# Kernel tuning notes

Hardware: AMD Instinct MI355X
Metric: run time of the kernel (lower is better)

## Reference

```python
import jax, jax.numpy as jnp
import numpy as np

B = 32          # batch_size
M = 1024        # mesh_num (nodes per sub-graph)
D_IN = 128      # sub_node_feature_input_dim
D_OUT = 128     # sub_node_feature_output_dim
E_DIM = 64      # embedding dim per node


def setup_inputs() -> dict:
    key = jax.random.key(0)
    k1, k2, k3, k4 = jax.random.split(key, 4)
    return {
        "node_feature_group": jax.random.normal(k1, (B * M, D_IN), dtype=jnp.float32),
        "embedding_group": jax.random.normal(k2, (B * M, E_DIM), dtype=jnp.float32),
        "W1": jax.random.normal(k3, (D_OUT, D_IN), dtype=jnp.float32) * (1.0 / np.sqrt(D_IN)),
        "W2": jax.random.normal(k4, (D_OUT, D_OUT), dtype=jnp.float32) * (1.0 / np.sqrt(D_OUT)),
    }


def reference(node_feature_group, embedding_group, W1, W2):
    # The torch module builds a (B*M)x(B*M) block-diagonal adjacency via
    # torch.block_diag; off-block entries are exactly zero, and row sums /
    # D^-1/2 A D^-1/2 normalization act per block, so we compute per-graph.
    E = embedding_group.reshape(B, M, E_DIM)
    adj = jnp.maximum(jnp.einsum('bme,bne->bmn', E, E), 0.0)  # clamp(E E^T, 0)
    adj = adj + jnp.eye(M, dtype=adj.dtype)                   # A = adj + I
    d = adj.sum(-1)                                           # [B, M]
    dinv = d ** -0.5                                          # symmetric=True
    dad = dinv[:, :, None] * adj * dinv[:, None, :]           # D^-1/2 A D^-1/2

    X = node_feature_group.reshape(B, M, D_IN)
    y = jax.nn.relu(jnp.einsum('bmn,bnd->bmd', dad, X) @ W1.T)   # gcn1
    y = jax.nn.relu(jnp.einsum('bmn,bnd->bmd', dad, y) @ W2.T)   # gcn2
    # Dropout is identity in eval mode.
    return y.reshape(B * M, D_OUT)
```

## Files before the change

### kernel.cpp

```cpp
#include <hip/hip_runtime.h>
#include <stdint.h>

#define B_  32
#define M_  1024
#define DF  128
#define ED  64

typedef __attribute__((ext_vector_type(8))) short short8;
typedef __attribute__((ext_vector_type(4))) short short4v;
typedef __attribute__((ext_vector_type(4))) float floatx4;

__device__ inline unsigned short f2bf(float f) {
    union { float f; unsigned u; } v; v.f = f;
    unsigned r = v.u + 0x7fffu + ((v.u >> 16) & 1u);
    return (unsigned short)(r >> 16);
}

__device__ inline short8 cvt8(float4 a, float4 b) {
    short8 s;
    s[0] = (short)f2bf(a.x); s[1] = (short)f2bf(a.y);
    s[2] = (short)f2bf(a.z); s[3] = (short)f2bf(a.w);
    s[4] = (short)f2bf(b.x); s[5] = (short)f2bf(b.y);
    s[6] = (short)f2bf(b.z); s[7] = (short)f2bf(b.w);
    return s;
}

__device__ inline void remap_block(int& b, int& mt2) {
    int lin = blockIdx.y * 16 + blockIdx.x;
    int g = lin & 7, kk = lin >> 3;
    b = g * 4 + (kk >> 4);
    mt2 = kk & 15;
}

__global__ __launch_bounds__(256) void prep_kernel(
    const float* __restrict__ E, const float* __restrict__ X,
    unsigned short* __restrict__ Ebf, float* __restrict__ dinv,
    unsigned short* __restrict__ Xt) {
    int b, mt2; remap_block(b, mt2);
    int m0 = mt2 * 64;
    int t = threadIdx.x;
    int w = t >> 6, lane = t & 63, quad = lane >> 4, lc = lane & 15;

    __shared__ unsigned short sEn[128 * 72];
    __shared__ float sDinv[64];

    const float* Eb = E + (size_t)b * M_ * ED;
    unsigned short* Ebg = Ebf + (size_t)b * M_ * ED;
    int base_m = m0 + w * 16;

    short8 afr[2];
    for (int ks = 0; ks < 2; ++ks) {
        const float* p = Eb + (size_t)(base_m + lc) * ED + ks * 32 + quad * 8;
        afr[ks] = cvt8(*(const float4*)p, *(const float4*)(p + 4));
    }
    floatx4 rsum = (floatx4){0.f, 0.f, 0.f, 0.f};

    for (int nc = 0; nc < 8; ++nc) {
        __syncthreads();
        for (int it = 0; it < 4; ++it) {
            int c = t + 256 * it;
            int row = c >> 3, off = (c & 7) * 8;
            const float* p = Eb + (size_t)(nc * 128 + row) * ED + off;
            *(short8*)(&sEn[row * 72 + off]) = cvt8(*(const float4*)p, *(const float4*)(p + 4));
        }
        __syncthreads();
        if ((mt2 & 7) == nc) {
            int half = mt2 >> 3;
            for (int it = 0; it < 2; ++it) {
                int c = t + 256 * it;
                int row = half * 64 + (c >> 3), off = (c & 7) * 8;
                *(short8*)(Ebg + (size_t)(nc * 128 + row) * ED + off) =
                    *(const short8*)(&sEn[row * 72 + off]);
            }
        }
        for (int nt = 0; nt < 8; ++nt) {
            short8 b0 = *(const short8*)(&sEn[(nt * 16 + lc) * 72 + quad * 8]);
            short8 b1 = *(const short8*)(&sEn[(nt * 16 + lc) * 72 + 32 + quad * 8]);
            floatx4 s = (floatx4){0.f, 0.f, 0.f, 0.f};
            s = __builtin_amdgcn_mfma_f32_16x16x32_bf16(afr[0], b0, s, 0, 0, 0);
            s = __builtin_amdgcn_mfma_f32_16x16x32_bf16(afr[1], b1, s, 0, 0, 0);
            int n = nc * 128 + nt * 16 + lc;
            for (int r = 0; r < 4; ++r) {
                int m = base_m + quad * 4 + r;
                float v = fmaxf(s[r], 0.f);
                if (m == n) v += 1.0f;
                rsum[r] += v;
            }
        }
    }
    for (int r = 0; r < 4; ++r) {
        float v = rsum[r];
        v += __shfl_xor(v, 1, 16);
        v += __shfl_xor(v, 2, 16);
        v += __shfl_xor(v, 4, 16);
        v += __shfl_xor(v, 8, 16);
        if (lc == 0) {
            float dvv = rsqrtf(v);
            int mloc = w * 16 + quad * 4 + r;
            sDinv[mloc] = dvv;
            dinv[b * M_ + m0 + mloc] = dvv;
        }
    }
    __syncthreads();
    {
        int nloc = t >> 5;
        int d4 = (t & 31) * 4;
        for (int pass = 0; pass < 8; ++pass) {
            int n = pass * 8 + nloc;
            float sc = sDinv[n];
            float4 v = *(const float4*)(X + (size_t)(b * M_ + m0 + n) * DF + d4);
            sEn[(d4 + 0) * 72 + n] = f2bf(v.x * sc);
            sEn[(d4 + 1) * 72 + n] = f2bf(v.y * sc);
            sEn[(d4 + 2) * 72 + n] = f2bf(v.z * sc);
            sEn[(d4 + 3) * 72 + n] = f2bf(v.w * sc);
        }
    }
    __syncthreads();
    for (int it = 0; it < 4; ++it) {
        int c = t + 256 * it;
        int d = c >> 3, off = (c & 7) * 8;
        *(short8*)(Xt + (size_t)(b * DF + d) * M_ + m0 + off) =
            *(const short8*)(&sEn[d * 72 + off]);
    }
}

template <int MODE>
__global__ __launch_bounds__(256) void layer_kernel(
    const unsigned short* __restrict__ Ebf,
    const unsigned short* __restrict__ Pt,
    const float* __restrict__ Wf,
    const float* __restrict__ dinv,
    unsigned short* __restrict__ OutT,
    float* __restrict__ OutF) {
    int b, mt2; remap_block(b, mt2);
    int m0 = mt2 * 64;
    int t = threadIdx.x;
    int w = t >> 6, lane = t & 63, quad = lane >> 4, lc = lane & 15;
    int wr = w & 1, wc = w >> 1;

    __shared__ unsigned short lds[35328];
    unsigned short* sEn = lds;
    unsigned short* sS  = lds + 9216;
    unsigned short* sPW = lds + 17920;

    const unsigned short* Eb = Ebf + (size_t)b * M_ * ED;
    const unsigned short* Pb = Pt + (size_t)b * DF * M_;

    short8 ae[2][2];
    for (int i = 0; i < 2; ++i) {
        int row = m0 + wr * 32 + i * 16 + lc;
        for (int ks = 0; ks < 2; ++ks)
            ae[i][ks] = *(const short8*)(Eb + (size_t)row * ED + ks * 32 + quad * 8);
    }

    floatx4 acc[2][4];
    for (int i = 0; i < 2; ++i)
        for (int j = 0; j < 4; ++j) acc[i][j] = (floatx4){0.f, 0.f, 0.f, 0.f};

    for (int nc = 0; nc < 8; ++nc) {
        __syncthreads();
        for (int it = 0; it < 4; ++it) {
            int c = t + 256 * it;
            int row = c >> 3, off = (c & 7) * 8;
            *(short8*)(&sEn[row * 72 + off]) =
                *(const short8*)(Eb + (size_t)(nc * 128 + row) * ED + off);
        }
        for (int it = 0; it < 8; ++it) {
            int c = t + 256 * it;
            int drow = c >> 4, off = (c & 15) * 8;
            *(short8*)(&sPW[drow * 136 + off]) =
                *(const short8*)(Pb + (size_t)drow * M_ + nc * 128 + off);
        }
        __syncthreads();
        for (int jt = 0; jt < 4; ++jt) {
            int ncol = wc * 64 + jt * 16;
            short8 b0 = *(const short8*)(&sEn[(ncol + lc) * 72 + quad * 8]);
            short8 b1 = *(const short8*)(&sEn[(ncol + lc) * 72 + 32 + quad * 8]);
            for (int i = 0; i < 2; ++i) {
                floatx4 s = (floatx4){0.f, 0.f, 0.f, 0.f};
                s = __builtin_amdgcn_mfma_f32_16x16x32_bf16(ae[i][0], b0, s, 0, 0, 0);
                s = __builtin_amdgcn_mfma_f32_16x16x32_bf16(ae[i][1], b1, s, 0, 0, 0);
                int mrow = wr * 32 + i * 16 + quad * 4;
                for (int r = 0; r < 4; ++r) {
                    float v = fmaxf(s[r], 0.f);
                    if (m0 + mrow + r == nc * 128 + ncol + lc) v += 1.0f;
                    sS[(mrow + r) * 136 + ncol + lc] = f2bf(v);
                }
            }
        }
        __syncthreads();
        for (int ks = 0; ks < 4; ++ks) {
            short8 afr[2], bfr[4];
            for (int i = 0; i < 2; ++i)
                afr[i] = *(const short8*)(&sS[(wr * 32 + i * 16 + lc) * 136 + ks * 32 + quad * 8]);
            for (int j = 0; j < 4; ++j)
                bfr[j] = *(const short8*)(&sPW[(wc * 64 + j * 16 + lc) * 136 + ks * 32 + quad * 8]);
            for (int i = 0; i < 2; ++i)
                for (int j = 0; j < 4; ++j)
                    acc[i][j] = __builtin_amdgcn_mfma_f32_16x16x32_bf16(afr[i], bfr[j], acc[i][j], 0, 0, 0);
        }
    }

    float dv[2][4];
    for (int i = 0; i < 2; ++i)
        for (int r = 0; r < 4; ++r)
            dv[i][r] = dinv[b * M_ + m0 + wr * 32 + i * 16 + quad * 4 + r];
    __syncthreads();
    unsigned short* sY = sS;
    unsigned short* sW = sPW;
    for (int i = 0; i < 2; ++i)
        for (int j = 0; j < 4; ++j) {
            int mrow = wr * 32 + i * 16 + quad * 4;
            int col = wc * 64 + j * 16 + lc;
            for (int r = 0; r < 4; ++r)
                sY[(mrow + r) * 136 + col] = f2bf(acc[i][j][r] * dv[i][r]);
        }
    for (int it = 0; it < 8; ++it) {
        int c = t + 256 * it;
        int row = c >> 4, off = (c & 15) * 8;
        const float* p = Wf + row * DF + off;
        *(short8*)(&sW[row * 136 + off]) = cvt8(*(const float4*)p, *(const float4*)(p + 4));
    }
    __syncthreads();
    floatx4 accH[2][4];
    for (int i = 0; i < 2; ++i)
        for (int j = 0; j < 4; ++j) accH[i][j] = (floatx4){0.f, 0.f, 0.f, 0.f};
    for (int ks = 0; ks < 4; ++ks) {
        short8 afr[2], bfr[4];
        for (int i = 0; i < 2; ++i)
            afr[i] = *(const short8*)(&sY[(wr * 32 + i * 16 + lc) * 136 + ks * 32 + quad * 8]);
        for (int j = 0; j < 4; ++j)
            bfr[j] = *(const short8*)(&sW[(wc * 64 + j * 16 + lc) * 136 + ks * 32 + quad * 8]);
        for (int i = 0; i < 2; ++i)
            for (int j = 0; j < 4; ++j)
                accH[i][j] = __builtin_amdgcn_mfma_f32_16x16x32_bf16(afr[i], bfr[j], accH[i][j], 0, 0, 0);
    }
    if (MODE == 2) {
        __syncthreads();
        float* sF = (float*)lds;
        for (int i = 0; i < 2; ++i)
            for (int j = 0; j < 4; ++j) {
                int mrow = wr * 32 + i * 16 + quad * 4;
                int col = wc * 64 + j * 16 + lc;
                for (int r = 0; r < 4; ++r)
                    sF[(mrow + r) * 132 + col] = fmaxf(accH[i][j][r], 0.f);
            }
        __syncthreads();
        float* Ob = OutF + ((size_t)b * M_ + m0) * DF;
        for (int it = 0; it < 8; ++it) {
            int c = t + 256 * it;
            int row = c >> 5, off = (c & 31) * 4;
            *(float4*)(Ob + (size_t)row * DF + off) = *(const float4*)(&sF[row * 132 + off]);
        }
    } else {
        __syncthreads();
        unsigned short* sT = sW;
        for (int i = 0; i < 2; ++i)
            for (int j = 0; j < 4; ++j) {
                int mrow = wr * 32 + i * 16 + quad * 4;
                int col = wc * 64 + j * 16 + lc;
                short4v pk;
                for (int r = 0; r < 4; ++r)
                    pk[r] = (short)f2bf(fmaxf(accH[i][j][r], 0.f) * dv[i][r]);
                *(short4v*)(&sT[col * 72 + mrow]) = pk;
            }
        __syncthreads();
        for (int it = 0; it < 4; ++it) {
            int c = t + 256 * it;
            int o = c >> 3, off = (c & 7) * 8;
            *(short8*)(OutT + (size_t)(b * DF + o) * M_ + m0 + off) =
                *(const short8*)(&sT[o * 72 + off]);
        }
    }
}

__global__ __launch_bounds__(256) void cast_kernel(
    const float* __restrict__ E, const float* __restrict__ W1,
    const float* __restrict__ W2, unsigned short* __restrict__ Ebf,
    unsigned short* __restrict__ W1bf, unsigned short* __restrict__ W2bf) {
    const int NE = B_ * M_ * ED;
    const int NW = DF * DF;
    int idx = (blockIdx.x * 256 + threadIdx.x) * 4;
    const float* src; unsigned short* dst; int off;
    if (idx < NE)            { src = E;  dst = Ebf;  off = idx; }
    else if (idx < NE + NW)  { src = W1; dst = W1bf; off = idx - NE; }
    else                     { src = W2; dst = W2bf; off = idx - NE - NW; }
    float4 v = *(const float4*)(src + off);
    ushort4 o;
    o.x = f2bf(v.x); o.y = f2bf(v.y); o.z = f2bf(v.z); o.w = f2bf(v.w);
    *(ushort4*)(dst + off) = o;
}

__global__ __launch_bounds__(256) void degree_kernel(
    const unsigned short* __restrict__ Ebf, float* __restrict__ dinv) {
    int mt = blockIdx.x, b = blockIdx.y;
    int t = threadIdx.x;
    int w = t >> 6, lane = t & 63, quad = lane >> 4, lc = lane & 15;
    __shared__ unsigned short sEn[128][72];
    const unsigned short* Eb = Ebf + (size_t)b * M_ * ED;
    short8 afr[2][2];
    for (int i = 0; i < 2; ++i) {
        int row = mt * 128 + w * 32 + i * 16 + lc;
        for (int ks = 0; ks < 2; ++ks)
            afr[i][ks] = *(const short8*)(Eb + (size_t)row * ED + ks * 32 + quad * 8);
    }
    floatx4 rsum[2];
    rsum[0] = (floatx4){0.f,0.f,0.f,0.f};
    rsum[1] = (floatx4){0.f,0.f,0.f,0.f};
    for (int nc = 0; nc < 8; ++nc) {
        __syncthreads();
        for (int it = 0; it < 4; ++it) {
            int c = t + 256 * it;
            int row = c >> 3, off = (c & 7) * 8;
            *(short8*)(&sEn[row][off]) =
                *(const short8*)(Eb + (size_t)(nc * 128 + row) * ED + off);
        }
        __syncthreads();
        for (int nt = 0; nt < 8; ++nt) {
            short8 b0 = *(const short8*)(&sEn[nt * 16 + lc][quad * 8]);
            short8 b1 = *(const short8*)(&sEn[nt * 16 + lc][32 + quad * 8]);
            for (int i = 0; i < 2; ++i) {
                floatx4 s = (floatx4){0.f,0.f,0.f,0.f};
                s = __builtin_amdgcn_mfma_f32_16x16x32_bf16(afr[i][0], b0, s, 0, 0, 0);
                s = __builtin_amdgcn_mfma_f32_16x16x32_bf16(afr[i][1], b1, s, 0, 0, 0);
                for (int r = 0; r < 4; ++r) rsum[i][r] += fmaxf(s[r], 0.f);
            }
        }
    }
    for (int i = 0; i < 2; ++i)
        for (int r = 0; r < 4; ++r) {
            float v = rsum[i][r];
            v += __shfl_xor(v, 1, 16);
            v += __shfl_xor(v, 2, 16);
            v += __shfl_xor(v, 4, 16);
            v += __shfl_xor(v, 8, 16);
            if (lc == 0) {
                int row = mt * 128 + w * 32 + i * 16 + quad * 4 + r;
                dinv[b * M_ + row] = rsqrtf(1.0f + v);
            }
        }
}

__global__ __launch_bounds__(256) void tscale128_kernel(
    const float* __restrict__ X, const float* __restrict__ dinv,
    unsigned short* __restrict__ Xt) {
    int mt = blockIdx.x, b = blockIdx.y;
    int t = threadIdx.x;
    __shared__ unsigned short sT[128][136];
    int nloc = t >> 5;
    int d4 = (t & 31) * 4;
    for (int pass = 0; pass < 16; ++pass) {
        int n = pass * 8 + nloc;
        int grow = b * M_ + mt * 128 + n;
        float sc = dinv[grow];
        float4 v = *(const float4*)(X + (size_t)grow * DF + d4);
        sT[d4 + 0][n] = f2bf(v.x * sc);
        sT[d4 + 1][n] = f2bf(v.y * sc);
        sT[d4 + 2][n] = f2bf(v.z * sc);
        sT[d4 + 3][n] = f2bf(v.w * sc);
    }
    __syncthreads();
    for (int it = 0; it < 8; ++it) {
        int c = t + 256 * it;
        int d = c >> 4, off = (c & 15) * 8;
        *(short8*)(Xt + (size_t)(b * DF + d) * M_ + mt * 128 + off) =
            *(const short8*)(&sT[d][off]);
    }
}

template <int MODE>
__global__ __launch_bounds__(256) void gcn_kernel(
    const unsigned short* __restrict__ Ebf,
    const unsigned short* __restrict__ Pt,
    const unsigned short* __restrict__ Wbf,
    const float* __restrict__ dinv,
    unsigned short* __restrict__ OutT,
    float* __restrict__ OutF) {
    int mt = blockIdx.x, b = blockIdx.y;
    int t = threadIdx.x;
    int w = t >> 6, lane = t & 63, quad = lane >> 4, lc = lane & 15;
    int wr = w & 1, wc = w >> 1;
    __shared__ unsigned short sEn[128][72];
    __shared__ unsigned short sS[128][136];
    __shared__ unsigned short sPW[128][136];
    const unsigned short* Eb = Ebf + (size_t)b * M_ * ED;
    short8 ae[4][2];
    for (int i = 0; i < 4; ++i) {
        int row = mt * 128 + wr * 64 + i * 16 + lc;
        for (int ks = 0; ks < 2; ++ks)
            ae[i][ks] = *(const short8*)(Eb + (size_t)row * ED + ks * 32 + quad * 8);
    }
    floatx4 accZ[4][4];
    for (int i = 0; i < 4; ++i)
        for (int j = 0; j < 4; ++j) accZ[i][j] = (floatx4){0.f,0.f,0.f,0.f};
    for (int nc = 0; nc < 8; ++nc) {
        __syncthreads();
        for (int it = 0; it < 4; ++it) {
            int c = t + 256 * it;
            int row = c >> 3, off = (c & 7) * 8;
            *(short8*)(&sEn[row][off]) =
                *(const short8*)(Eb + (size_t)(nc * 128 + row) * ED + off);
        }
        for (int it = 0; it < 8; ++it) {
            int c = t + 256 * it;
            int drow = c >> 4, off = (c & 15) * 8;
            *(short8*)(&sPW[drow][off]) =
                *(const short8*)(Pt + (size_t)(b * DF + drow) * M_ + nc * 128 + off);
        }
        __syncthreads();
        for (int jt = 0; jt < 4; ++jt) {
            int ncol = wc * 64 + jt * 16;
            short8 b0 = *(const short8*)(&sEn[ncol + lc][quad * 8]);
            short8 b1 = *(const short8*)(&sEn[ncol + lc][32 + quad * 8]);
            for (int i = 0; i < 4; ++i) {
                floatx4 s = (floatx4){0.f,0.f,0.f,0.f};
                s = __builtin_amdgcn_mfma_f32_16x16x32_bf16(ae[i][0], b0, s, 0, 0, 0);
                s = __builtin_amdgcn_mfma_f32_16x16x32_bf16(ae[i][1], b1, s, 0, 0, 0);
                int mrow = wr * 64 + i * 16 + quad * 4;
                for (int r = 0; r < 4; ++r) {
                    float v = fmaxf(s[r], 0.f);
                    if (mt == nc && (mrow + r) == (ncol + lc)) v += 1.0f;
                    sS[mrow + r][ncol + lc] = f2bf(v);
                }
            }
        }
        __syncthreads();
        for (int ks = 0; ks < 4; ++ks) {
            short8 afr[4];
            for (int i = 0; i < 4; ++i)
                afr[i] = *(const short8*)(&sS[wr * 64 + i * 16 + lc][ks * 32 + quad * 8]);
            for (int j = 0; j < 4; ++j) {
                short8 bfr = *(const short8*)(&sPW[wc * 64 + j * 16 + lc][ks * 32 + quad * 8]);
                for (int i = 0; i < 4; ++i)
                    accZ[i][j] = __builtin_amdgcn_mfma_f32_16x16x32_bf16(afr[i], bfr, accZ[i][j], 0, 0, 0);
            }
        }
    }
    float dv[4][4];
    for (int i = 0; i < 4; ++i)
        for (int r = 0; r < 4; ++r)
            dv[i][r] = dinv[b * M_ + mt * 128 + wr * 64 + i * 16 + quad * 4 + r];
    __syncthreads();
    for (int i = 0; i < 4; ++i)
        for (int j = 0; j < 4; ++j) {
            int mrow = wr * 64 + i * 16 + quad * 4;
            int col = wc * 64 + j * 16 + lc;
            for (int r = 0; r < 4; ++r)
                sS[mrow + r][col] = f2bf(accZ[i][j][r] * dv[i][r]);
        }
    for (int it = 0; it < 8; ++it) {
        int c = t + 256 * it;
        int row = c >> 4, off = (c & 15) * 8;
        *(short8*)(&sPW[row][off]) = *(const short8*)(Wbf + row * DF + off);
    }
    __syncthreads();
    floatx4 accH[4][4];
    for (int i = 0; i < 4; ++i)
        for (int j = 0; j < 4; ++j) accH[i][j] = (floatx4){0.f,0.f,0.f,0.f};
    for (int ks = 0; ks < 4; ++ks) {
        short8 afr[4], bfr[4];
        for (int i = 0; i < 4; ++i)
            afr[i] = *(const short8*)(&sS[wr * 64 + i * 16 + lc][ks * 32 + quad * 8]);
        for (int j = 0; j < 4; ++j)
            bfr[j] = *(const short8*)(&sPW[wc * 64 + j * 16 + lc][ks * 32 + quad * 8]);
        for (int i = 0; i < 4; ++i)
            for (int j = 0; j < 4; ++j)
                accH[i][j] = __builtin_amdgcn_mfma_f32_16x16x32_bf16(afr[i], bfr[j], accH[i][j], 0, 0, 0);
    }
    if (MODE == 2) {
        float* Ob = OutF + ((size_t)b * M_ + mt * 128) * DF;
        for (int i = 0; i < 4; ++i)
            for (int j = 0; j < 4; ++j) {
                int mrow = wr * 64 + i * 16 + quad * 4;
                int col = wc * 64 + j * 16 + lc;
                for (int r = 0; r < 4; ++r)
                    Ob[(size_t)(mrow + r) * DF + col] = fmaxf(accH[i][j][r], 0.f);
            }
    } else {
        __syncthreads();
        for (int i = 0; i < 4; ++i)
            for (int j = 0; j < 4; ++j) {
                int mrow = wr * 64 + i * 16 + quad * 4;
                int col = wc * 64 + j * 16 + lc;
                for (int r = 0; r < 4; ++r)
                    sS[col][mrow + r] = f2bf(fmaxf(accH[i][j][r], 0.f) * dv[i][r]);
            }
        __syncthreads();
        unsigned short* Ob = OutT + (size_t)b * DF * M_ + mt * 128;
        for (int it = 0; it < 8; ++it) {
            int c = t + 256 * it;
            int orow = c >> 4, off = (c & 15) * 8;
            *(short8*)(Ob + (size_t)orow * M_ + off) = *(const short8*)(&sS[orow][off]);
        }
    }
}

extern "C" void kernel_launch(void* const* d_in, const int* in_sizes, int n_in,
                              void* d_out, int out_size, void* d_ws, size_t ws_size,
                              hipStream_t stream) {
    (void)in_sizes; (void)n_in; (void)out_size;
    const float* X  = (const float*)d_in[0];
    const float* E  = (const float*)d_in[1];
    const float* W1 = (const float*)d_in[2];
    const float* W2 = (const float*)d_in[3];
    float* out = (float*)d_out;

    char* ws = (char*)d_ws;
    unsigned short* Ebf  = (unsigned short*)(ws);
    unsigned short* W1bf = (unsigned short*)(ws + 4194304);
    unsigned short* W2bf = (unsigned short*)(ws + 4227072);
    float*          dinv = (float*)(ws + 4259840);
    unsigned short* Xt   = (unsigned short*)(ws + 4390912);
    unsigned short* Ht   = (unsigned short*)(ws + 12779520);
    const size_t NEED = 21168128ull;

    if (ws_size >= NEED) {
        prep_kernel<<<dim3(16, 32), 256, 0, stream>>>(E, X, Ebf, dinv, Xt);
        layer_kernel<1><<<dim3(16, 32), 256, 0, stream>>>(Ebf, Xt, W1, dinv, Ht, nullptr);
        layer_kernel<2><<<dim3(16, 32), 256, 0, stream>>>(Ebf, Ht, W2, dinv, nullptr, out);
    } else {
        cast_kernel<<<2080, 256, 0, stream>>>(E, W1, W2, Ebf, W1bf, W2bf);
        degree_kernel<<<dim3(8, 32), 256, 0, stream>>>(Ebf, dinv);
        tscale128_kernel<<<dim3(8, 32), 256, 0, stream>>>(X, dinv, Xt);
        gcn_kernel<1><<<dim3(8, 32), 256, 0, stream>>>(Ebf, Xt, W1bf, dinv, Ht, nullptr);
        gcn_kernel<2><<<dim3(8, 32), 256, 0, stream>>>(Ebf, Ht, W2bf, dinv, nullptr, out);
    }
}
```

Measured before the change: 154.1 us.

## Fuse prep and both GCN layers into one kernel with per-graph atomic barriers

Merges the prep kernel and the two layer kernels into a single persistent-style launch. Blocks belonging to the same graph synchronise through a global atomic counter spin barrier between stages. Each block keeps its dinv values and its E fragments in registers and LDS, so they are not re-read from global memory. This removes two kernel launches and their tail gaps, but adds a memset and spin-wait overhead. The barrier relies on all 512 blocks being co-resident (launch bounds 256,2); if they are not, the kernel can deadlock.

After: 222.2 us. 44.2% more time.

```diff
diff --git a/kernel.cpp b/kernel.cpp
--- a/kernel.cpp
+++ b/kernel.cpp
@@ -32,127 +32,28 @@
     mt2 = kk & 15;
 }
 
-__global__ __launch_bounds__(256) void prep_kernel(
-    const float* __restrict__ E, const float* __restrict__ X,
-    unsigned short* __restrict__ Ebf, float* __restrict__ dinv,
-    unsigned short* __restrict__ Xt) {
-    int b, mt2; remap_block(b, mt2);
-    int m0 = mt2 * 64;
-    int t = threadIdx.x;
-    int w = t >> 6, lane = t & 63, quad = lane >> 4, lc = lane & 15;
-
-    __shared__ unsigned short sEn[128 * 72];
-    __shared__ float sDinv[64];
-
-    const float* Eb = E + (size_t)b * M_ * ED;
-    unsigned short* Ebg = Ebf + (size_t)b * M_ * ED;
-    int base_m = m0 + w * 16;
-
-    short8 afr[2];
-    for (int ks = 0; ks < 2; ++ks) {
-        const float* p = Eb + (size_t)(base_m + lc) * ED + ks * 32 + quad * 8;
-        afr[ks] = cvt8(*(const float4*)p, *(const float4*)(p + 4));
-    }
-    floatx4 rsum = (floatx4){0.f, 0.f, 0.f, 0.f};
-
-    for (int nc = 0; nc < 8; ++nc) {
-        __syncthreads();
-        for (int it = 0; it < 4; ++it) {
-            int c = t + 256 * it;
-            int row = c >> 3, off = (c & 7) * 8;
-            const float* p = Eb + (size_t)(nc * 128 + row) * ED + off;
-            *(short8*)(&sEn[row * 72 + off]) = cvt8(*(const float4*)p, *(const float4*)(p + 4));
-        }
-        __syncthreads();
-        if ((mt2 & 7) == nc) {
-            int half = mt2 >> 3;
-            for (int it = 0; it < 2; ++it) {
-                int c = t + 256 * it;
-                int row = half * 64 + (c >> 3), off = (c & 7) * 8;
-                *(short8*)(Ebg + (size_t)(nc * 128 + row) * ED + off) =
-                    *(const short8*)(&sEn[row * 72 + off]);
-            }
-        }
-        for (int nt = 0; nt < 8; ++nt) {
-            short8 b0 = *(const short8*)(&sEn[(nt * 16 + lc) * 72 + quad * 8]);
-            short8 b1 = *(const short8*)(&sEn[(nt * 16 + lc) * 72 + 32 + quad * 8]);
-            floatx4 s = (floatx4){0.f, 0.f, 0.f, 0.f};
-            s = __builtin_amdgcn_mfma_f32_16x16x32_bf16(afr[0], b0, s, 0, 0, 0);
-            s = __builtin_amdgcn_mfma_f32_16x16x32_bf16(afr[1], b1, s, 0, 0, 0);
-            int n = nc * 128 + nt * 16 + lc;
-            for (int r = 0; r < 4; ++r) {
-                int m = base_m + quad * 4 + r;
-                float v = fmaxf(s[r], 0.f);
-                if (m == n) v += 1.0f;
-                rsum[r] += v;
-            }
-        }
-    }
-    for (int r = 0; r < 4; ++r) {
-        float v = rsum[r];
-        v += __shfl_xor(v, 1, 16);
-        v += __shfl_xor(v, 2, 16);
-        v += __shfl_xor(v, 4, 16);
-        v += __shfl_xor(v, 8, 16);
-        if (lc == 0) {
-            float dvv = rsqrtf(v);
-            int mloc = w * 16 + quad * 4 + r;
-            sDinv[mloc] = dvv;
-            dinv[b * M_ + m0 + mloc] = dvv;
-        }
-    }
-    __syncthreads();
-    {
-        int nloc = t >> 5;
-        int d4 = (t & 31) * 4;
-        for (int pass = 0; pass < 8; ++pass) {
-            int n = pass * 8 + nloc;
-            float sc = sDinv[n];
-            float4 v = *(const float4*)(X + (size_t)(b * M_ + m0 + n) * DF + d4);
-            sEn[(d4 + 0) * 72 + n] = f2bf(v.x * sc);
-            sEn[(d4 + 1) * 72 + n] = f2bf(v.y * sc);
-            sEn[(d4 + 2) * 72 + n] = f2bf(v.z * sc);
-            sEn[(d4 + 3) * 72 + n] = f2bf(v.w * sc);
-        }
-    }
-    __syncthreads();
-    for (int it = 0; it < 4; ++it) {
-        int c = t + 256 * it;
-        int d = c >> 3, off = (c & 7) * 8;
-        *(short8*)(Xt + (size_t)(b * DF + d) * M_ + m0 + off) =
-            *(const short8*)(&sEn[d * 72 + off]);
-    }
+__device__ inline void graph_barrier(unsigned* c, unsigned target) {
+    __syncthreads();
+    if (threadIdx.x == 0) {
+        __threadfence();
+        atomicAdd(c, 1u);
+        while (atomicAdd(c, 0u) < target)
+            __builtin_amdgcn_s_sleep(8);
+        __threadfence();
+    }
+    __syncthreads();
 }
 
 template <int MODE>
-__global__ __launch_bounds__(256) void layer_kernel(
-    const unsigned short* __restrict__ Ebf,
-    const unsigned short* __restrict__ Pt,
+__device__ __forceinline__ void layer_body(
+    int m0, int t, int quad, int lc, int wr, int wc,
+    const short8 (&ae)[2][2], const float (&dv)[2][4],
+    const unsigned short* __restrict__ Eb,
+    const unsigned short* __restrict__ Pb,
     const float* __restrict__ Wf,
-    const float* __restrict__ dinv,
-    unsigned short* __restrict__ OutT,
-    float* __restrict__ OutF) {
-    int b, mt2; remap_block(b, mt2);
-    int m0 = mt2 * 64;
-    int t = threadIdx.x;
-    int w = t >> 6, lane = t & 63, quad = lane >> 4, lc = lane & 15;
-    int wr = w & 1, wc = w >> 1;
-
-    __shared__ unsigned short lds[35328];
-    unsigned short* sEn = lds;
-    unsigned short* sS  = lds + 9216;
-    unsigned short* sPW = lds + 17920;
-
-    const unsigned short* Eb = Ebf + (size_t)b * M_ * ED;
-    const unsigned short* Pb = Pt + (size_t)b * DF * M_;
-
-    short8 ae[2][2];
-    for (int i = 0; i < 2; ++i) {
-        int row = m0 + wr * 32 + i * 16 + lc;
-        for (int ks = 0; ks < 2; ++ks)
-            ae[i][ks] = *(const short8*)(Eb + (size_t)row * ED + ks * 32 + quad * 8);
-    }
-
+    unsigned short* sEn, unsigned short* sS, unsigned short* sPW,
+    unsigned short* __restrict__ OtB,
+    float* __restrict__ OfB) {
     floatx4 acc[2][4];
     for (int i = 0; i < 2; ++i)
         for (int j = 0; j < 4; ++j) acc[i][j] = (floatx4){0.f, 0.f, 0.f, 0.f};
@@ -201,10 +102,6 @@
         }
     }
 
-    float dv[2][4];
-    for (int i = 0; i < 2; ++i)
-        for (int r = 0; r < 4; ++r)
-            dv[i][r] = dinv[b * M_ + m0 + wr * 32 + i * 16 + quad * 4 + r];
     __syncthreads();
     unsigned short* sY = sS;
     unsigned short* sW = sPW;
@@ -237,7 +134,7 @@
     }
     if (MODE == 2) {
         __syncthreads();
-        float* sF = (float*)lds;
+        float* sF = (float*)sEn;
         for (int i = 0; i < 2; ++i)
             for (int j = 0; j < 4; ++j) {
                 int mrow = wr * 32 + i * 16 + quad * 4;
@@ -246,7 +143,7 @@
                     sF[(mrow + r) * 132 + col] = fmaxf(accH[i][j][r], 0.f);
             }
         __syncthreads();
-        float* Ob = OutF + ((size_t)b * M_ + m0) * DF;
+        float* Ob = OfB + (size_t)m0 * DF;
         for (int it = 0; it < 8; ++it) {
             int c = t + 256 * it;
             int row = c >> 5, off = (c & 31) * 4;
@@ -268,10 +165,126 @@
         for (int it = 0; it < 4; ++it) {
             int c = t + 256 * it;
             int o = c >> 3, off = (c & 7) * 8;
-            *(short8*)(OutT + (size_t)(b * DF + o) * M_ + m0 + off) =
+            *(short8*)(OtB + (size_t)o * M_ + m0 + off) =
                 *(const short8*)(&sT[o * 72 + off]);
         }
     }
+}
+
+__global__ __launch_bounds__(256, 2) void fused_kernel(
+    const float* __restrict__ E, const float* __restrict__ X,
+    const float* __restrict__ W1f, const float* __restrict__ W2f,
+    unsigned short* __restrict__ Ebf, unsigned short* __restrict__ Xt,
+    unsigned short* __restrict__ Ht, unsigned* __restrict__ cnt,
+    float* __restrict__ out) {
+    int b, mt2; remap_block(b, mt2);
+    int m0 = mt2 * 64;
+    int t = threadIdx.x;
+    int w = t >> 6, lane = t & 63, quad = lane >> 4, lc = lane & 15;
+    int wr = w & 1, wc = w >> 1;
+
+    __shared__ unsigned short lds[35328];
+    __shared__ float sDinv[64];
+    unsigned short* sEn = lds;
+    unsigned short* sS  = lds + 9216;
+    unsigned short* sPW = lds + 17920;
+
+    const float* Eb = E + (size_t)b * M_ * ED;
+    unsigned short* Ebg = Ebf + (size_t)b * M_ * ED;
+
+    short8 ae[2][2];
+    {
+        int base_m = m0 + w * 16;
+        short8 afr[2];
+        for (int ks = 0; ks < 2; ++ks) {
+            const float* p = Eb + (size_t)(base_m + lc) * ED + ks * 32 + quad * 8;
+            afr[ks] = cvt8(*(const float4*)p, *(const float4*)(p + 4));
+        }
+        floatx4 rsum = (floatx4){0.f, 0.f, 0.f, 0.f};
+        for (int nc = 0; nc < 8; ++nc) {
+            __syncthreads();
+            for (int it = 0; it < 4; ++it) {
+                int c = t + 256 * it;
+                int row = c >> 3, off = (c & 7) * 8;
+                const float* p = Eb + (size_t)(nc * 128 + row) * ED + off;
+                *(short8*)(&sEn[row * 72 + off]) = cvt8(*(const float4*)p, *(const float4*)(p + 4));
+            }
+            __syncthreads();
+            if ((mt2 & 7) == nc) {
+                int half = mt2 >> 3;
+                for (int it = 0; it < 2; ++it) {
+                    int c = t + 256 * it;
+                    int row = half * 64 + (c >> 3), off = (c & 7) * 8;
+                    *(short8*)(Ebg + (size_t)(nc * 128 + row) * ED + off) =
+                        *(const short8*)(&sEn[row * 72 + off]);
+                }
+            }
+            if (nc == (mt2 >> 1)) {
+                int rl = (mt2 & 1) * 64 + wr * 32 + lc;
+                for (int i = 0; i < 2; ++i)
+                    for (int ks = 0; ks < 2; ++ks)
+                        ae[i][ks] = *(const short8*)(&sEn[(rl + i * 16) * 72 + ks * 32 + quad * 8]);
+            }
+            for (int nt = 0; nt < 8; ++nt) {
+                short8 b0 = *(const short8*)(&sEn[(nt * 16 + lc) * 72 + quad * 8]);
+                short8 b1 = *(const short8*)(&sEn[(nt * 16 + lc) * 72 + 32 + quad * 8]);
+                floatx4 s = (floatx4){0.f, 0.f, 0.f, 0.f};
+                s = __builtin_amdgcn_mfma_f32_16x16x32_bf16(afr[0], b0, s, 0, 0, 0);
+                s = __builtin_amdgcn_mfma_f32_16x16x32_bf16(afr[1], b1, s, 0, 0, 0);
+                int n = nc * 128 + nt * 16 + lc;
+                for (int r = 0; r < 4; ++r) {
+                    int m = base_m + quad * 4 + r;
+                    float v = fmaxf(s[r], 0.f);
+                    if (m == n) v += 1.0f;
+                    rsum[r] += v;
+                }
+            }
+        }
+        for (int r = 0; r < 4; ++r) {
+            float v = rsum[r];
+            v += __shfl_xor(v, 1, 16);
+            v += __shfl_xor(v, 2, 16);
+            v += __shfl_xor(v, 4, 16);
+            v += __shfl_xor(v, 8, 16);
+            if (lc == 0) sDinv[w * 16 + quad * 4 + r] = rsqrtf(v);
+        }
+        __syncthreads();
+    }
+    float dv[2][4];
+    for (int i = 0; i < 2; ++i)
+        for (int r = 0; r < 4; ++r)
+            dv[i][r] = sDinv[wr * 32 + i * 16 + quad * 4 + r];
+    {
+        int nloc = t >> 5;
+        int d4 = (t & 31) * 4;
+        for (int pass = 0; pass < 8; ++pass) {
+            int n = pass * 8 + nloc;
+            float sc = sDinv[n];
+            float4 v = *(const float4*)(X + (size_t)(b * M_ + m0 + n) * DF + d4);
+            sEn[(d4 + 0) * 72 + n] = f2bf(v.x * sc);
+            sEn[(d4 + 1) * 72 + n] = f2bf(v.y * sc);
+            sEn[(d4 + 2) * 72 + n] = f2bf(v.z * sc);
+            sEn[(d4 + 3) * 72 + n] = f2bf(v.w * sc);
+        }
+    }
+    __syncthreads();
+    for (int it = 0; it < 4; ++it) {
+        int c = t + 256 * it;
+        int d = c >> 3, off = (c & 7) * 8;
+        *(short8*)(Xt + (size_t)(b * DF + d) * M_ + m0 + off) =
+            *(const short8*)(&sEn[d * 72 + off]);
+    }
+
+    unsigned* cb = cnt + b;
+    const unsigned short* EbB = Ebf + (size_t)b * M_ * ED;
+    graph_barrier(cb, 16);
+    layer_body<1>(m0, t, quad, lc, wr, wc, ae, dv,
+                  EbB, Xt + (size_t)b * DF * M_, W1f,
+                  sEn, sS, sPW, Ht + (size_t)b * DF * M_, nullptr);
+    graph_barrier(cb, 32);
+    layer_body<2>(m0, t, quad, lc, wr, wc, ae, dv,
+                  EbB, Ht + (size_t)b * DF * M_, W2f,
+                  sEn, sS, sPW, nullptr, out + (size_t)b * M_ * DF);
 }
 
 __global__ __launch_bounds__(256) void cast_kernel(
@@ -512,12 +525,12 @@
     float*          dinv = (float*)(ws + 4259840);
     unsigned short* Xt   = (unsigned short*)(ws + 4390912);
     unsigned short* Ht   = (unsigned short*)(ws + 12779520);
-    const size_t NEED = 21168128ull;
+    unsigned*       cnt  = (unsigned*)(ws + 21168128);
+    const size_t NEED = 21168128ull + 128ull;
 
     if (ws_size >= NEED) {
-        prep_kernel<<<dim3(16, 32), 256, 0, stream>>>(E, X, Ebf, dinv, Xt);
-        layer_kernel<1><<<dim3(16, 32), 256, 0, stream>>>(Ebf, Xt, W1, dinv, Ht, nullptr);
-        layer_kernel<2><<<dim3(16, 32), 256, 0, stream>>>(Ebf, Ht, W2, dinv, nullptr, out);
+        hipMemsetAsync(cnt, 0, B_ * sizeof(unsigned), stream);
+        fused_kernel<<<dim3(16, 32), 256, 0, stream>>>(E, X, W1, W2, Ebf, Xt, Ht, cnt, out);
     } else {
         cast_kernel<<<2080, 256, 0, stream>>>(E, W1, W2, Ebf, W1bf, W2bf);
         degree_kernel<<<dim3(8, 32), 256, 0, stream>>>(Ebf, dinv);
```

## Split layer kernel across 8 waves with XOR-swizzled 64KB LDS tiles

Applied to the files above, without the earlier changes.

The layer kernel now runs with 512 threads (8 waves) instead of 256. Each wave owns a 16x64 output slice rather than 32x64, so per-wave accumulator registers halve and more waves are available to hide latency. The padded LDS arrays are replaced by a byte-addressed 64KB buffer with XOR-swizzled row layouts for the E, S and P/W tiles, meant to avoid bank conflicts without padding. The larger LDS footprint limits how many blocks fit per CU. The A-fragment reuse within each wave also drops, so more LDS and global fragment loads happen per MFMA.

Result: no change. 156.7 us (+1.7%).

```diff
diff --git a/kernel.cpp b/kernel.cpp
--- a/kernel.cpp
+++ b/kernel.cpp
@@ -31,6 +31,10 @@
     b = g * 4 + (kk >> 4);
     mt2 = kk & 15;
 }
+
+#define SEN(row, colb) (        (row) * 128 + (((colb)) ^ (((row) & 7) << 4)))
+#define SSB(row, colb) (16384 + (row) * 256 + (((colb)) ^ (((row) & 7) << 4)))
+#define SPW(row, colb) (32768 + (row) * 256 + (((colb)) ^ (((row) & 7) << 4)))
 
 __global__ __launch_bounds__(256) void prep_kernel(
     const float* __restrict__ E, const float* __restrict__ X,
@@ -125,7 +129,7 @@
 }
 
 template <int MODE>
-__global__ __launch_bounds__(256) void layer_kernel(
+__global__ __launch_bounds__(512, 4) void layer_kernel(
     const unsigned short* __restrict__ Ebf,
     const unsigned short* __restrict__ Pt,
     const float* __restrict__ Wf,
@@ -136,137 +140,121 @@
     int m0 = mt2 * 64;
     int t = threadIdx.x;
     int w = t >> 6, lane = t & 63, quad = lane >> 4, lc = lane & 15;
-    int wr = w & 1, wc = w >> 1;
-
-    __shared__ unsigned short lds[35328];
-    unsigned short* sEn = lds;
-    unsigned short* sS  = lds + 9216;
-    unsigned short* sPW = lds + 17920;
+    int wr = w >> 1, wc = w & 1;
+
+    __shared__ char lds[65536];
 
     const unsigned short* Eb = Ebf + (size_t)b * M_ * ED;
     const unsigned short* Pb = Pt + (size_t)b * DF * M_;
 
-    short8 ae[2][2];
-    for (int i = 0; i < 2; ++i) {
-        int row = m0 + wr * 32 + i * 16 + lc;
+    short8 ae[2];
+    {
+        int row = m0 + wr * 16 + lc;
         for (int ks = 0; ks < 2; ++ks)
-            ae[i][ks] = *(const short8*)(Eb + (size_t)row * ED + ks * 32 + quad * 8);
-    }
-
-    floatx4 acc[2][4];
-    for (int i = 0; i < 2; ++i)
-        for (int j = 0; j < 4; ++j) acc[i][j] = (floatx4){0.f, 0.f, 0.f, 0.f};
+            ae[ks] = *(const short8*)(Eb + (size_t)row * ED + ks * 32 + quad * 8);
+    }
+    float dv[4];
+    for (int r = 0; r < 4; ++r)
+        dv[r] = dinv[b * M_ + m0 + wr * 16 + quad * 4 + r];
+
+    floatx4 acc[4];
+    for (int j = 0; j < 4; ++j) acc[j] = (floatx4){0.f, 0.f, 0.f, 0.f};
 
     for (int nc = 0; nc < 8; ++nc) {
         __syncthreads();
+        for (int it = 0; it < 2; ++it) {
+            int c = t + 512 * it;
+            int row = c >> 3, colb = (c & 7) * 16;
+            *(short8*)(lds + SEN(row, colb)) =
+                *(const short8*)(Eb + (size_t)(nc * 128 + row) * ED + (c & 7) * 8);
+        }
         for (int it = 0; it < 4; ++it) {
-            int c = t + 256 * it;
-            int row = c >> 3, off = (c & 7) * 8;
-            *(short8*)(&sEn[row * 72 + off]) =
-                *(const short8*)(Eb + (size_t)(nc * 128 + row) * ED + off);
-        }
-        for (int it = 0; it < 8; ++it) {
-            int c = t + 256 * it;
-            int drow = c >> 4, off = (c & 15) * 8;
-            *(short8*)(&sPW[drow * 136 + off]) =
-                *(const short8*)(Pb + (size_t)drow * M_ + nc * 128 + off);
+            int c = t + 512 * it;
+            int row = c >> 4, colb = (c & 15) * 16;
+            *(short8*)(lds + SPW(row, colb)) =
+                *(const short8*)(Pb + (size_t)row * M_ + nc * 128 + (c & 15) * 8);
         }
         __syncthreads();
         for (int jt = 0; jt < 4; ++jt) {
             int ncol = wc * 64 + jt * 16;
-            short8 b0 = *(const short8*)(&sEn[(ncol + lc) * 72 + quad * 8]);
-            short8 b1 = *(const short8*)(&sEn[(ncol + lc) * 72 + 32 + quad * 8]);
-            for (int i = 0; i < 2; ++i) {
-                floatx4 s = (floatx4){0.f, 0.f, 0.f, 0.f};
-                s = __builtin_amdgcn_mfma_f32_16x16x32_bf16(ae[i][0], b0, s, 0, 0, 0);
-                s = __builtin_amdgcn_mfma_f32_16x16x32_bf16(ae[i][1], b1, s, 0, 0, 0);
-                int mrow = wr * 32 + i * 16 + quad * 4;
-                for (int r = 0; r < 4; ++r) {
-                    float v = fmaxf(s[r], 0.f);
-                    if (m0 + mrow + r == nc * 128 + ncol + lc) v += 1.0f;
-                    sS[(mrow + r) * 136 + ncol + lc] = f2bf(v);
-                }
+            short8 b0 = *(const short8*)(lds + SEN(ncol + lc, quad * 16));
+            short8 b1 = *(const short8*)(lds + SEN(ncol + lc, 64 + quad * 16));
+            floatx4 s = (floatx4){0.f, 0.f, 0.f, 0.f};
+            s = __builtin_amdgcn_mfma_f32_16x16x32_bf16(ae[0], b0, s, 0, 0, 0);
+            s = __builtin_amdgcn_mfma_f32_16x16x32_bf16(ae[1], b1, s, 0, 0, 0);
+            for (int r = 0; r < 4; ++r) {
+                int mloc = wr * 16 + quad * 4 + r;
+                int nloc = ncol + lc;
+                float v = fmaxf(s[r], 0.f);
+                if (m0 + mloc == nc * 128 + nloc) v += 1.0f;
+                *(unsigned short*)(lds + SSB(mloc, 2 * nloc)) = f2bf(v);
             }
         }
         __syncthreads();
         for (int ks = 0; ks < 4; ++ks) {
-            short8 afr[2], bfr[4];
-            for (int i = 0; i < 2; ++i)
-                afr[i] = *(const short8*)(&sS[(wr * 32 + i * 16 + lc) * 136 + ks * 32 + quad * 8]);
-            for (int j = 0; j < 4; ++j)
-                bfr[j] = *(const short8*)(&sPW[(wc * 64 + j * 16 + lc) * 136 + ks * 32 + quad * 8]);
-            for (int i = 0; i < 2; ++i)
-                for (int j = 0; j < 4; ++j)
-                    acc[i][j] = __builtin_amdgcn_mfma_f32_16x16x32_bf16(afr[i], bfr[j], acc[i][j], 0, 0, 0);
-        }
-    }
-
-    float dv[2][4];
-    for (int i = 0; i < 2; ++i)
-        for (int r = 0; r < 4; ++r)
-            dv[i][r] = dinv[b * M_ + m0 + wr * 32 + i * 16 + quad * 4 + r];
-    __syncthreads();
-    unsigned short* sY = sS;
-    unsigned short* sW = sPW;
-    for (int i = 0; i < 2; ++i)
+            short8 afr = *(const short8*)(lds + SSB(wr * 16 + lc, ks * 64 + quad * 16));
+            for (int j = 0; j < 4; ++j) {
+                short8 bfr = *(const short8*)(lds + SPW(wc * 64 + j * 16 + lc, ks * 64 + quad * 16));
+                acc[j] = __builtin_amdgcn_mfma_f32_16x16x32_bf16(afr, bfr, acc[j], 0, 0, 0);
+            }
+        }
+    }
+
+    __syncthreads();
+    for (int j = 0; j < 4; ++j) {
+        int col = wc * 64 + j * 16 + lc;
+        for (int r = 0; r < 4; ++r) {
+            int mloc = wr * 16 + quad * 4 + r;
+            *(unsigned short*)(lds + SSB(mloc, 2 * col)) = f2bf(acc[j][r] * dv[r]);
+        }
+    }
+    for (int it = 0; it < 4; ++it) {
+        int c = t + 512 * it;
+        int row = c >> 4, colb = (c & 15) * 16;
+        const float* p = Wf + row * DF + (c & 15) * 8;
+        *(short8*)(lds + SPW(row, colb)) = cvt8(*(const float4*)p, *(const float4*)(p + 4));
+    }
+    __syncthreads();
+    floatx4 accH[4];
+    for (int j = 0; j < 4; ++j) accH[j] = (floatx4){0.f, 0.f, 0.f, 0.f};
+    for (int ks = 0; ks < 4; ++ks) {
+        short8 afr = *(const short8*)(lds + SSB(wr * 16 + lc, ks * 64 + quad * 16));
         for (int j = 0; j < 4; ++j) {
-            int mrow = wr * 32 + i * 16 + quad * 4;
+            short8 bfr = *(const short8*)(lds + SPW(wc * 64 + j * 16 + lc, ks * 64 + quad * 16));
+            accH[j] = __builtin_amdgcn_mfma_f32_16x16x32_bf16(afr, bfr, accH[j], 0, 0, 0);
+        }
+    }
+    if (MODE == 2) {
+        __syncthreads();
+        float* sF = (float*)lds;
+        for (int j = 0; j < 4; ++j) {
             int col = wc * 64 + j * 16 + lc;
-            for (int r = 0; r < 4; ++r)
-                sY[(mrow + r) * 136 + col] = f2bf(acc[i][j][r] * dv[i][r]);
-        }
-    for (int it = 0; it < 8; ++it) {
-        int c = t + 256 * it;
-        int row = c >> 4, off = (c & 15) * 8;
-        const float* p = Wf + row * DF + off;
-        *(short8*)(&sW[row * 136 + off]) = cvt8(*(const float4*)p, *(const float4*)(p + 4));
-    }
-    __syncthreads();
-    floatx4 accH[2][4];
-    for (int i = 0; i < 2; ++i)
-        for (int j = 0; j < 4; ++j) accH[i][j] = (floatx4){0.f, 0.f, 0.f, 0.f};
-    for (int ks = 0; ks < 4; ++ks) {
-        short8 afr[2], bfr[4];
-        for (int i = 0; i < 2; ++i)
-            afr[i] = *(const short8*)(&sY[(wr * 32 + i * 16 + lc) * 136 + ks * 32 + quad * 8]);
-        for (int j = 0; j < 4; ++j)
-            bfr[j] = *(const short8*)(&sW[(wc * 64 + j * 16 + lc) * 136 + ks * 32 + quad * 8]);
-        for (int i = 0; i < 2; ++i)
-            for (int j = 0; j < 4; ++j)
-                accH[i][j] = __builtin_amdgcn_mfma_f32_16x16x32_bf16(afr[i], bfr[j], accH[i][j], 0, 0, 0);
-    }
-    if (MODE == 2) {
-        __syncthreads();
-        float* sF = (float*)lds;
-        for (int i = 0; i < 2; ++i)
-            for (int j = 0; j < 4; ++j) {
-                int mrow = wr * 32 + i * 16 + quad * 4;
-                int col = wc * 64 + j * 16 + lc;
-                for (int r = 0; r < 4; ++r)
-                    sF[(mrow + r) * 132 + col] = fmaxf(accH[i][j][r], 0.f);
-            }
+            for (int r = 0; r < 4; ++r) {
+                int mloc = wr * 16 + quad * 4 + r;
+                sF[mloc * 132 + col] = fmaxf(accH[j][r], 0.f);
+            }
+        }
         __syncthreads();
         float* Ob = OutF + ((size_t)b * M_ + m0) * DF;
-        for (int it = 0; it < 8; ++it) {
-            int c = t + 256 * it;
+        for (int it = 0; it < 4; ++it) {
+            int c = t + 512 * it;
             int row = c >> 5, off = (c & 31) * 4;
             *(float4*)(Ob + (size_t)row * DF + off) = *(const float4*)(&sF[row * 132 + off]);
         }
     } else {
         __syncthreads();
-        unsigned short* sT = sW;
-        for (int i = 0; i < 2; ++i)
-            for (int j = 0; j < 4; ++j) {
-                int mrow = wr * 32 + i * 16 + quad * 4;
-                int col = wc * 64 + j * 16 + lc;
-                short4v pk;
-                for (int r = 0; r < 4; ++r)
-                    pk[r] = (short)f2bf(fmaxf(accH[i][j][r], 0.f) * dv[i][r]);
-                *(short4v*)(&sT[col * 72 + mrow]) = pk;
-            }
-        __syncthreads();
-        for (int it = 0; it < 4; ++it) {
-            int c = t + 256 * it;
+        unsigned short* sT = (unsigned short*)lds;
+        for (int j = 0; j < 4; ++j) {
+            int col = wc * 64 + j * 16 + lc;
+            int mloc = wr * 16 + quad * 4;
+            short4v pk;
+            for (int r = 0; r < 4; ++r)
+                pk[r] = (short)f2bf(fmaxf(accH[j][r], 0.f) * dv[r]);
+            *(short4v*)(&sT[col * 72 + mloc]) = pk;
+        }
+        __syncthreads();
+        for (int it = 0; it < 2; ++it) {
+            int c = t + 512 * it;
             int o = c >> 3, off = (c & 7) * 8;
             *(short8*)(OutT + (size_t)(b * DF + o) * M_ + m0 + off) =
                 *(const short8*)(&sT[o * 72 + off]);
@@ -516,8 +504,8 @@
 
     if (ws_size >= NEED) {
         prep_kernel<<<dim3(16, 32), 256, 0, stream>>>(E, X, Ebf, dinv, Xt);
-        layer_kernel<1><<<dim3(16, 32), 256, 0, stream>>>(Ebf, Xt, W1, dinv, Ht, nullptr);
-        layer_kernel<2><<<dim3(16, 32), 256, 0, stream>>>(Ebf, Ht, W2, dinv, nullptr, out);
+        layer_kernel<1><<<dim3(16, 32), 512, 0, stream>>>(Ebf, Xt, W1, dinv, Ht, nullptr);
+        layer_kernel<2><<<dim3(16, 32), 512, 0, stream>>>(Ebf, Ht, W2, dinv, nullptr, out);
     } else {
         cast_kernel<<<2080, 256, 0, stream>>>(E, W1, W2, Ebf, W1bf, W2bf);
         degree_kernel<<<dim3(8, 32), 256, 0, stream>>>(Ebf, dinv);
```

## Double-buffer layer tiles via direct global-to-LDS loads with 128-row blocks

Applied to the files above, without the earlier changes.

The layer kernel now runs 512-thread blocks that each cover 128 rows instead of 64, so every staged chunk of E and the transposed features serves twice as many output rows. Chunks are loaded with global_load_lds (direct global-to-LDS DMA) into two LDS buffers, fetching the next chunk while the current one is being computed, and one barrier per iteration is removed. To match the DMA's contiguous layout, the LDS row padding is dropped, which can cause bank conflicts on fragment reads. The 128 KB of LDS allows only one block per CU, and the grid now has 256 blocks.

Measured after the change: 181.1 us. 17.5% more time.

```diff
diff --git a/kernel.cpp b/kernel.cpp
--- a/kernel.cpp
+++ b/kernel.cpp
@@ -23,6 +23,12 @@
     s[4] = (short)f2bf(b.x); s[5] = (short)f2bf(b.y);
     s[6] = (short)f2bf(b.z); s[7] = (short)f2bf(b.w);
     return s;
+}
+
+__device__ inline void load_lds16(const void* g, void* l) {
+    __builtin_amdgcn_global_load_lds(
+        (const __attribute__((address_space(1))) unsigned int*)g,
+        (__attribute__((address_space(3))) unsigned int*)l, 16, 0, 0);
 }
 
 __device__ inline void remap_block(int& b, int& mt2) {
@@ -125,23 +131,21 @@
 }
 
 template <int MODE>
-__global__ __launch_bounds__(256) void layer_kernel(
+__global__ __launch_bounds__(512, 2) void layer_kernel(
     const unsigned short* __restrict__ Ebf,
     const unsigned short* __restrict__ Pt,
     const float* __restrict__ Wf,
     const float* __restrict__ dinv,
     unsigned short* __restrict__ OutT,
     float* __restrict__ OutF) {
-    int b, mt2; remap_block(b, mt2);
-    int m0 = mt2 * 64;
+    int b = blockIdx.x, mt = blockIdx.y;
+    int m0 = mt * 128;
     int t = threadIdx.x;
     int w = t >> 6, lane = t & 63, quad = lane >> 4, lc = lane & 15;
-    int wr = w & 1, wc = w >> 1;
-
-    __shared__ unsigned short lds[35328];
-    unsigned short* sEn = lds;
-    unsigned short* sS  = lds + 9216;
-    unsigned short* sPW = lds + 17920;
+    int wr = w >> 1, wc = w & 1;
+
+    __shared__ char lds[131072];
+    unsigned short* sS = (unsigned short*)(lds + 32768);
 
     const unsigned short* Eb = Ebf + (size_t)b * M_ * ED;
     const unsigned short* Pb = Pt + (size_t)b * DF * M_;
@@ -152,39 +156,51 @@
         for (int ks = 0; ks < 2; ++ks)
             ae[i][ks] = *(const short8*)(Eb + (size_t)row * ED + ks * 32 + quad * 8);
     }
+    float dv[2][4];
+    for (int i = 0; i < 2; ++i)
+        for (int r = 0; r < 4; ++r)
+            dv[i][r] = dinv[b * M_ + m0 + wr * 32 + i * 16 + quad * 4 + r];
 
     floatx4 acc[2][4];
     for (int i = 0; i < 2; ++i)
         for (int j = 0; j < 4; ++j) acc[i][j] = (floatx4){0.f, 0.f, 0.f, 0.f};
 
+    auto stage = [&](int sel, int nc) {
+        for (int r = 0; r < 2; ++r) {
+            int slot = r * 8 + w;
+            int te = slot * 64 + lane;
+            const void* gp = Eb + (size_t)(nc * 128 + (te >> 3)) * ED + (te & 7) * 8;
+            load_lds16(gp, lds + sel * 16384 + slot * 1024);
+        }
+        for (int r = 0; r < 4; ++r) {
+            int slot = r * 8 + w;
+            int te = slot * 64 + lane;
+            const void* gp = Pb + (size_t)(te >> 4) * M_ + nc * 128 + (te & 15) * 8;
+            load_lds16(gp, lds + 65536 + sel * 32768 + slot * 1024);
+        }
+    };
+
+    int cur = 0;
+    stage(0, 0);
+    __syncthreads();
+
     for (int nc = 0; nc < 8; ++nc) {
-        __syncthreads();
-        for (int it = 0; it < 4; ++it) {
-            int c = t + 256 * it;
-            int row = c >> 3, off = (c & 7) * 8;
-            *(short8*)(&sEn[row * 72 + off]) =
-                *(const short8*)(Eb + (size_t)(nc * 128 + row) * ED + off);
-        }
-        for (int it = 0; it < 8; ++it) {
-            int c = t + 256 * it;
-            int drow = c >> 4, off = (c & 15) * 8;
-            *(short8*)(&sPW[drow * 136 + off]) =
-                *(const short8*)(Pb + (size_t)drow * M_ + nc * 128 + off);
-        }
-        __syncthreads();
+        if (nc < 7) stage(cur ^ 1, nc + 1);
+        const unsigned short* sEn = (const unsigned short*)(lds + cur * 16384);
+        const unsigned short* sPW = (const unsigned short*)(lds + 65536 + cur * 32768);
         for (int jt = 0; jt < 4; ++jt) {
             int ncol = wc * 64 + jt * 16;
-            short8 b0 = *(const short8*)(&sEn[(ncol + lc) * 72 + quad * 8]);
-            short8 b1 = *(const short8*)(&sEn[(ncol + lc) * 72 + 32 + quad * 8]);
+            short8 b0 = *(const short8*)(&sEn[(ncol + lc) * 64 + quad * 8]);
+            short8 b1 = *(const short8*)(&sEn[(ncol + lc) * 64 + 32 + quad * 8]);
             for (int i = 0; i < 2; ++i) {
                 floatx4 s = (floatx4){0.f, 0.f, 0.f, 0.f};
                 s = __builtin_amdgcn_mfma_f32_16x16x32_bf16(ae[i][0], b0, s, 0, 0, 0);
                 s = __builtin_amdgcn_mfma_f32_16x16x32_bf16(ae[i][1], b1, s, 0, 0, 0);
-                int mrow = wr * 32 + i * 16 + quad * 4;
+                int mloc = wr * 32 + i * 16 + quad * 4;
                 for (int r = 0; r < 4; ++r) {
                     float v = fmaxf(s[r], 0.f);
-                    if (m0 + mrow + r == nc * 128 + ncol + lc) v += 1.0f;
-                    sS[(mrow + r) * 136 + ncol + lc] = f2bf(v);
+                    if (m0 + mloc + r == nc * 128 + ncol + lc) v += 1.0f;
+                    sS[(mloc + r) * 128 + ncol + lc] = f2bf(v);
                 }
             }
         }
@@ -192,34 +208,31 @@
         for (int ks = 0; ks < 4; ++ks) {
             short8 afr[2], bfr[4];
             for (int i = 0; i < 2; ++i)
-                afr[i] = *(const short8*)(&sS[(wr * 32 + i * 16 + lc) * 136 + ks * 32 + quad * 8]);
+                afr[i] = *(const short8*)(&sS[(wr * 32 + i * 16 + lc) * 128 + ks * 32 + quad * 8]);
             for (int j = 0; j < 4; ++j)
-                bfr[j] = *(const short8*)(&sPW[(wc * 64 + j * 16 + lc) * 136 + ks * 32 + quad * 8]);
+                bfr[j] = *(const short8*)(&sPW[(wc * 64 + j * 16 + lc) * 128 + ks * 32 + quad * 8]);
             for (int i = 0; i < 2; ++i)
                 for (int j = 0; j < 4; ++j)
                     acc[i][j] = __builtin_amdgcn_mfma_f32_16x16x32_bf16(afr[i], bfr[j], acc[i][j], 0, 0, 0);
         }
-    }
-
-    float dv[2][4];
-    for (int i = 0; i < 2; ++i)
-        for (int r = 0; r < 4; ++r)
-            dv[i][r] = dinv[b * M_ + m0 + wr * 32 + i * 16 + quad * 4 + r];
-    __syncthreads();
+        __syncthreads();
+        cur ^= 1;
+    }
+
     unsigned short* sY = sS;
-    unsigned short* sW = sPW;
+    unsigned short* sW = (unsigned short*)(lds + 65536);
     for (int i = 0; i < 2; ++i)
         for (int j = 0; j < 4; ++j) {
             int mrow = wr * 32 + i * 16 + quad * 4;
             int col = wc * 64 + j * 16 + lc;
             for (int r = 0; r < 4; ++r)
-                sY[(mrow + r) * 136 + col] = f2bf(acc[i][j][r] * dv[i][r]);
-        }
-    for (int it = 0; it < 8; ++it) {
-        int c = t + 256 * it;
+                sY[(mrow + r) * 128 + col] = f2bf(acc[i][j][r] * dv[i][r]);
+        }
+    for (int it = 0; it < 4; ++it) {
+        int c = t + 512 * it;
         int row = c >> 4, off = (c & 15) * 8;
         const float* p = Wf + row * DF + off;
-        *(short8*)(&sW[row * 136 + off]) = cvt8(*(const float4*)p, *(const float4*)(p + 4));
+        *(short8*)(&sW[row * 128 + off]) = cvt8(*(const float4*)p, *(const float4*)(p + 4));
     }
     __syncthreads();
     floatx4 accH[2][4];
@@ -228,9 +241,9 @@
     for (int ks = 0; ks < 4; ++ks) {
         short8 afr[2], bfr[4];
         for (int i = 0; i < 2; ++i)
-            afr[i] = *(const short8*)(&sY[(wr * 32 + i * 16 + lc) * 136 + ks * 32 + quad * 8]);
+            afr[i] = *(const short8*)(&sY[(wr * 32 + i * 16 + lc) * 128 + ks * 32 + quad * 8]);
         for (int j = 0; j < 4; ++j)
-            bfr[j] = *(const short8*)(&sW[(wc * 64 + j * 16 + lc) * 136 + ks * 32 + quad * 8]);
+            bfr[j] = *(const short8*)(&sW[(wc * 64 + j * 16 + lc) * 128 + ks * 32 + quad * 8]);
         for (int i = 0; i < 2; ++i)
             for (int j = 0; j < 4; ++j)
                 accH[i][j] = __builtin_amdgcn_mfma_f32_16x16x32_bf16(afr[i], bfr[j], accH[i][j], 0, 0, 0);
@@ -248,13 +261,13 @@
         __syncthreads();
         float* Ob = OutF + ((size_t)b * M_ + m0) * DF;
         for (int it = 0; it < 8; ++it) {
-            int c = t + 256 * it;
+            int c = t + 512 * it;
             int row = c >> 5, off = (c & 31) * 4;
             *(float4*)(Ob + (size_t)row * DF + off) = *(const float4*)(&sF[row * 132 + off]);
         }
     } else {
         __syncthreads();
-        unsigned short* sT = sW;
+        unsigned short* sT = (unsigned short*)lds;
         for (int i = 0; i < 2; ++i)
             for (int j = 0; j < 4; ++j) {
                 int mrow = wr * 32 + i * 16 + quad * 4;
@@ -262,14 +275,14 @@
                 short4v pk;
                 for (int r = 0; r < 4; ++r)
                     pk[r] = (short)f2bf(fmaxf(accH[i][j][r], 0.f) * dv[i][r]);
-                *(short4v*)(&sT[col * 72 + mrow]) = pk;
+                *(short4v*)(&sT[col * 136 + mrow]) = pk;
             }
         __syncthreads();
         for (int it = 0; it < 4; ++it) {
-            int c = t + 256 * it;
-            int o = c >> 3, off = (c & 7) * 8;
+            int c = t + 512 * it;
+            int o = c >> 4, off = (c & 15) * 8;
             *(short8*)(OutT + (size_t)(b * DF + o) * M_ + m0 + off) =
-                *(const short8*)(&sT[o * 72 + off]);
+                *(const short8*)(&sT[o * 136 + off]);
         }
     }
 }
@@ -516,8 +529,8 @@
 
     if (ws_size >= NEED) {
         prep_kernel<<<dim3(16, 32), 256, 0, stream>>>(E, X, Ebf, dinv, Xt);
-        layer_kernel<1><<<dim3(16, 32), 256, 0, stream>>>(Ebf, Xt, W1, dinv, Ht, nullptr);
-        layer_kernel<2><<<dim3(16, 32), 256, 0, stream>>>(Ebf, Ht, W2, dinv, nullptr, out);
+        layer_kernel<1><<<dim3(32, 8), 512, 0, stream>>>(Ebf, Xt, W1, dinv, Ht, nullptr);
+        layer_kernel<2><<<dim3(32, 8), 512, 0, stream>>>(Ebf, Ht, W2, dinv, nullptr, out);
     } else {
         cast_kernel<<<2080, 256, 0, stream>>>(E, W1, W2, Ebf, W1bf, W2bf);
         degree_kernel<<<dim3(8, 32), 256, 0, stream>>>(Ebf, dinv);
```
